# Performance work log

Measured on AMD Instinct MI355X. Metric: run time of the kernel, lower is better.

## Reference

```python
import jax, jax.numpy as jnp
import numpy as np

EPS = 1e-5

def _ln(x, g, b):
    mu = x.mean(-1, keepdims=True)
    var = ((x - mu) ** 2).mean(-1, keepdims=True)
    return (x - mu) / jnp.sqrt(var + EPS) * g + b

def setup_inputs() -> dict:
    key = jax.random.key(0)
    ks = jax.random.split(key, 24)
    B, S, I, H, D, F = 64, 512, 32, 64, 128, 256
    def w(k, shape, fan_in):
        return jax.random.uniform(k, shape, jnp.float32, -1.0, 1.0) / np.sqrt(fan_in)
    return {
        'x': jax.random.normal(ks[0], (B, S, I), jnp.float32),
        'W_ih': w(ks[1], (H, I), H), 'b_ih': w(ks[2], (H,), H),
        'W_hh': w(ks[3], (H, H), H), 'b_hh': w(ks[4], (H,), H),
        'Wp': w(ks[5], (D, H), H), 'bp': w(ks[6], (D,), H),
        'Wqkv': w(ks[7], (3 * D, D), D), 'bqkv': jnp.zeros((3 * D,), jnp.float32),
        'Wo': w(ks[8], (D, D), D), 'bo': jnp.zeros((D,), jnp.float32),
        'g1': jnp.ones((D,), jnp.float32), 'be1': jnp.zeros((D,), jnp.float32),
        'W1': w(ks[9], (F, D), D), 'b1': w(ks[10], (F,), D),
        'W2': w(ks[11], (D, F), F), 'b2': w(ks[12], (D,), F),
        'g2': jnp.ones((D,), jnp.float32), 'be2': jnp.zeros((D,), jnp.float32),
        'gn': jnp.ones((D,), jnp.float32), 'bn': jnp.zeros((D,), jnp.float32),
        'Wf': w(ks[13], (I, D), D), 'bf': w(ks[14], (I,), D),
    }

def reference(x, W_ih, b_ih, W_hh, b_hh, Wp, bp, Wqkv, bqkv, Wo, bo,
              g1, be1, W1, b1, W2, b2, g2, be2, gn, bn, Wf, bf):
    B, S, I = x.shape
    H = W_ih.shape[0]
    D = Wp.shape[0]
    nh = 8
    hd = D // nh

    # RNNCell tanh recurrence over time (sequential, vectorized over batch)
    xs = jnp.swapaxes(x, 0, 1)  # (S, B, I)
    def step(h, x_t):
        h = jnp.tanh(x_t @ W_ih.T + b_ih + h @ W_hh.T + b_hh)
        return h, h
    _, hs = jax.lax.scan(step, jnp.zeros((B, H), x.dtype), xs)  # (S, B, H)

    proj = hs @ Wp.T + bp  # (S, B, D)

    # TransformerEncoderLayer (post-norm, relu), dropout = identity (eval)
    qkv = proj @ Wqkv.T + bqkv  # (S, B, 3D)
    q, k, v = jnp.split(qkv, 3, axis=-1)
    q = q.reshape(S, B, nh, hd)
    k = k.reshape(S, B, nh, hd)
    v = v.reshape(S, B, nh, hd)
    scores = jnp.einsum('sbhd,tbhd->bhst', q, k) / np.sqrt(hd)
    attn = jax.nn.softmax(scores, axis=-1)
    ctx = jnp.einsum('bhst,tbhd->sbhd', attn, v).reshape(S, B, D)
    attn_out = ctx @ Wo.T + bo
    x1 = _ln(proj + attn_out, g1, be1)
    ff = jax.nn.relu(x1 @ W1.T + b1) @ W2.T + b2
    x2 = _ln(x1 + ff, g2, be2)

    out = _ln(x2 + proj, gn, bn)
    pooled = out.mean(axis=0)  # (B, D)
    return jnp.tanh(pooled @ Wf.T + bf)
```

## Files before the change

kernel.cpp:

```cpp
#include <hip/hip_runtime.h>
#include <hip/hip_bf16.h>

#define BB 64
#define SS 512
#define II 32
#define HH 64
#define DD 128
#define FF 256
#define NHEAD 8
#define HDIM 16
#define NTOK (SS*BB)

typedef short bf16x8 __attribute__((ext_vector_type(8)));
typedef float f32x4  __attribute__((ext_vector_type(4)));

__device__ __forceinline__ float fast_tanh(float x) {
    float ax = fabsf(x);
    float e = __expf(-2.0f * ax);
    float r = (1.0f - e) * __builtin_amdgcn_rcpf(1.0f + e);
    return copysignf(r, x);
}

__device__ __forceinline__ float bcast(float v, int lane) {
    return __int_as_float(__builtin_amdgcn_readlane(__float_as_int(v), lane));
}

__device__ __forceinline__ short f2bf(float x) {
    unsigned u = __float_as_uint(x);
    return (short)((u + 0x7FFFu + ((u >> 16) & 1u)) >> 16);
}

__global__ __launch_bounds__(256) void k_xw(const float* __restrict__ x,
                                            const float* __restrict__ W_ih,
                                            const float* __restrict__ b_ih,
                                            const float* __restrict__ b_hh,
                                            float* __restrict__ xw) {
    int idx = blockIdx.x * 256 + threadIdx.x;
    int j  = idx & (HH - 1);
    int sb = idx >> 6;
    int s  = sb >> 6;
    int b  = sb & (BB - 1);
    const float* xr = x + (b * SS + s) * II;
    const float* wr = W_ih + j * II;
    float acc = b_ih[j] + b_hh[j];
    #pragma unroll
    for (int k = 0; k < II; k += 4) {
        float4 xv = *(const float4*)(xr + k);
        float4 wv = *(const float4*)(wr + k);
        acc += xv.x * wv.x + xv.y * wv.y + xv.z * wv.z + xv.w * wv.w;
    }
    xw[idx] = acc;
}

__global__ __launch_bounds__(64, 1) void k_rnn(const float* __restrict__ xw,
                                               const float* __restrict__ W_hh,
                                               float* __restrict__ hs) {
    int b = blockIdx.x;
    int j = threadIdx.x;
    float w[HH];
    #pragma unroll
    for (int k = 0; k < HH; k++) w[k] = W_hh[j * HH + k];

    float hv = 0.0f;
    float xv0 = xw[(0 * BB + b) * HH + j];
    float xv1 = xw[(1 * BB + b) * HH + j];
    for (int t = 0; t < SS; t++) {
        int tn = (t < SS - 2) ? t + 2 : t;
        float xnext = xw[(tn * BB + b) * HH + j];
        float a0 = xv0, a1 = 0.f, a2 = 0.f, a3 = 0.f;
        #pragma unroll
        for (int k = 0; k < HH; k += 4) {
            a0 = fmaf(w[k + 0], bcast(hv, k + 0), a0);
            a1 = fmaf(w[k + 1], bcast(hv, k + 1), a1);
            a2 = fmaf(w[k + 2], bcast(hv, k + 2), a2);
            a3 = fmaf(w[k + 3], bcast(hv, k + 3), a3);
        }
        hv = fast_tanh((a0 + a1) + (a2 + a3));
        hs[(t * BB + b) * HH + j] = hv;
        xv0 = xv1;
        xv1 = xnext;
    }
}

template<int K, bool RELU>
__global__ __launch_bounds__(256) void k_gemm_m64(const float* __restrict__ A,
                                                  const float* __restrict__ W,
                                                  const float* __restrict__ bias,
                                                  float* __restrict__ C, int N) {
    __shared__ short As[64 * 40];
    __shared__ short Ws[128 * 40];
    int tid = threadIdx.x;
    int wid = tid >> 6, lane = tid & 63;
    int col = lane & 15, quad = lane >> 4;
    int rowBase = blockIdx.x * 64, colBase = blockIdx.y * 128;

    f32x4 acc[8];
    #pragma unroll
    for (int nt = 0; nt < 8; nt++) {
        float bv = bias[colBase + nt * 16 + col];
        acc[nt][0] = bv; acc[nt][1] = bv; acc[nt][2] = bv; acc[nt][3] = bv;
    }

    int arow = tid >> 2, akb = (tid & 3) * 8;
    int wrow = tid >> 1, wkb = (tid & 1) * 16;

    for (int kb = 0; kb < K; kb += 32) {
        {
            const float4* ap = (const float4*)(A + (size_t)(rowBase + arow) * K + kb + akb);
            float4 v0 = ap[0], v1 = ap[1];
            short t0[8];
            t0[0]=f2bf(v0.x); t0[1]=f2bf(v0.y); t0[2]=f2bf(v0.z); t0[3]=f2bf(v0.w);
            t0[4]=f2bf(v1.x); t0[5]=f2bf(v1.y); t0[6]=f2bf(v1.z); t0[7]=f2bf(v1.w);
            *(int4*)&As[arow * 40 + akb] = *(int4*)t0;
        }
        {
            const float4* wp = (const float4*)(W + (size_t)(colBase + wrow) * K + kb + wkb);
            float4 v0 = wp[0], v1 = wp[1], v2 = wp[2], v3 = wp[3];
            short t0[8], t1[8];
            t0[0]=f2bf(v0.x); t0[1]=f2bf(v0.y); t0[2]=f2bf(v0.z); t0[3]=f2bf(v0.w);
            t0[4]=f2bf(v1.x); t0[5]=f2bf(v1.y); t0[6]=f2bf(v1.z); t0[7]=f2bf(v1.w);
            t1[0]=f2bf(v2.x); t1[1]=f2bf(v2.y); t1[2]=f2bf(v2.z); t1[3]=f2bf(v2.w);
            t1[4]=f2bf(v3.x); t1[5]=f2bf(v3.y); t1[6]=f2bf(v3.z); t1[7]=f2bf(v3.w);
            *(int4*)&Ws[wrow * 40 + wkb]     = *(int4*)t0;
            *(int4*)&Ws[wrow * 40 + wkb + 8] = *(int4*)t1;
        }
        __syncthreads();

        bf16x8 af = *(const bf16x8*)&As[(wid * 16 + col) * 40 + quad * 8];
        bf16x8 wf[8];
        #pragma unroll
        for (int nt = 0; nt < 8; nt++)
            wf[nt] = *(const bf16x8*)&Ws[(nt * 16 + col) * 40 + quad * 8];
        #pragma unroll
        for (int nt = 0; nt < 8; nt++)
            acc[nt] = __builtin_amdgcn_mfma_f32_16x16x32_bf16(af, wf[nt], acc[nt], 0, 0, 0);
        __syncthreads();
    }

    #pragma unroll
    for (int r = 0; r < 4; r++) {
        int m = rowBase + wid * 16 + quad * 4 + r;
        float* crow = C + (size_t)m * N + colBase;
        #pragma unroll
        for (int nt = 0; nt < 8; nt++) {
            float v = acc[nt][r];
            if (RELU) v = fmaxf(v, 0.f);
            crow[nt * 16 + col] = v;
        }
    }
}

template<int K, int NLN>
__global__ __launch_bounds__(256) void k_gemm_ln_m64(const float* __restrict__ A,
                                                     const float* __restrict__ W,
                                                     const float* __restrict__ bias,
                                                     const float* __restrict__ res1,
                                                     const float* __restrict__ g1v,
                                                     const float* __restrict__ be1v,
                                                     const float* __restrict__ res2,
                                                     const float* __restrict__ g2v,
                                                     const float* __restrict__ be2v,
                                                     float* __restrict__ out) {
    __shared__ short As[64 * 40];
    __shared__ short Ws[128 * 40];
    int tid = threadIdx.x;
    int wid = tid >> 6, lane = tid & 63;
    int col = lane & 15, quad = lane >> 4;
    int rowBase = blockIdx.x * 64;

    f32x4 acc[8];
    #pragma unroll
    for (int nt = 0; nt < 8; nt++) {
        float bv = bias[nt * 16 + col];
        acc[nt][0] = bv; acc[nt][1] = bv; acc[nt][2] = bv; acc[nt][3] = bv;
    }

    int arow = tid >> 2, akb = (tid & 3) * 8;
    int wrow = tid >> 1, wkb = (tid & 1) * 16;

    for (int kb = 0; kb < K; kb += 32) {
        {
            const float4* ap = (const float4*)(A + (size_t)(rowBase + arow) * K + kb + akb);
            float4 v0 = ap[0], v1 = ap[1];
            short t0[8];
            t0[0]=f2bf(v0.x); t0[1]=f2bf(v0.y); t0[2]=f2bf(v0.z); t0[3]=f2bf(v0.w);
            t0[4]=f2bf(v1.x); t0[5]=f2bf(v1.y); t0[6]=f2bf(v1.z); t0[7]=f2bf(v1.w);
            *(int4*)&As[arow * 40 + akb] = *(int4*)t0;
        }
        {
            const float4* wp = (const float4*)(W + (size_t)wrow * K + kb + wkb);
            float4 v0 = wp[0], v1 = wp[1], v2 = wp[2], v3 = wp[3];
            short t0[8], t1[8];
            t0[0]=f2bf(v0.x); t0[1]=f2bf(v0.y); t0[2]=f2bf(v0.z); t0[3]=f2bf(v0.w);
            t0[4]=f2bf(v1.x); t0[5]=f2bf(v1.y); t0[6]=f2bf(v1.z); t0[7]=f2bf(v1.w);
            t1[0]=f2bf(v2.x); t1[1]=f2bf(v2.y); t1[2]=f2bf(v2.z); t1[3]=f2bf(v2.w);
            t1[4]=f2bf(v3.x); t1[5]=f2bf(v3.y); t1[6]=f2bf(v3.z); t1[7]=f2bf(v3.w);
            *(int4*)&Ws[wrow * 40 + wkb]     = *(int4*)t0;
            *(int4*)&Ws[wrow * 40 + wkb + 8] = *(int4*)t1;
        }
        __syncthreads();

        bf16x8 af = *(const bf16x8*)&As[(wid * 16 + col) * 40 + quad * 8];
        bf16x8 wf[8];
        #pragma unroll
        for (int nt = 0; nt < 8; nt++)
            wf[nt] = *(const bf16x8*)&Ws[(nt * 16 + col) * 40 + quad * 8];
        #pragma unroll
        for (int nt = 0; nt < 8; nt++)
            acc[nt] = __builtin_amdgcn_mfma_f32_16x16x32_bf16(af, wf[nt], acc[nt], 0, 0, 0);
        __syncthreads();
    }

    float ga[8], ba[8], gb[8], bb[8];
    #pragma unroll
    for (int nt = 0; nt < 8; nt++) {
        ga[nt] = g1v[nt * 16 + col]; ba[nt] = be1v[nt * 16 + col];
        if (NLN == 2) { gb[nt] = g2v[nt * 16 + col]; bb[nt] = be2v[nt * 16 + col]; }
    }

    #pragma unroll
    for (int r = 0; r < 4; r++) {
        int m = rowBase + wid * 16 + quad * 4 + r;
        const float* rr1 = res1 + (size_t)m * DD;
        float v[8];
        float s = 0.f;
        #pragma unroll
        for (int nt = 0; nt < 8; nt++) {
            v[nt] = acc[nt][r] + rr1[nt * 16 + col];
            s += v[nt];
        }
        #pragma unroll
        for (int off = 1; off < 16; off <<= 1) s += __shfl_xor(s, off, 64);
        float mu = s * (1.0f / 128.0f);
        float vs = 0.f;
        #pragma unroll
        for (int nt = 0; nt < 8; nt++) { v[nt] -= mu; vs += v[nt] * v[nt]; }
        #pragma unroll
        for (int off = 1; off < 16; off <<= 1) vs += __shfl_xor(vs, off, 64);
        float rstd = rsqrtf(vs * (1.0f / 128.0f) + 1e-5f);
        #pragma unroll
        for (int nt = 0; nt < 8; nt++) v[nt] = v[nt] * rstd * ga[nt] + ba[nt];

        if (NLN == 2) {
            const float* rr2 = res2 + (size_t)m * DD;
            float s2 = 0.f;
            #pragma unroll
            for (int nt = 0; nt < 8; nt++) {
                v[nt] += rr2[nt * 16 + col];
                s2 += v[nt];
            }
            #pragma unroll
            for (int off = 1; off < 16; off <<= 1) s2 += __shfl_xor(s2, off, 64);
            float mu2 = s2 * (1.0f / 128.0f);
            float vs2 = 0.f;
            #pragma unroll
            for (int nt = 0; nt < 8; nt++) { v[nt] -= mu2; vs2 += v[nt] * v[nt]; }
            #pragma unroll
            for (int off = 1; off < 16; off <<= 1) vs2 += __shfl_xor(vs2, off, 64);
            float rstd2 = rsqrtf(vs2 * (1.0f / 128.0f) + 1e-5f);
            #pragma unroll
            for (int nt = 0; nt < 8; nt++) v[nt] = v[nt] * rstd2 * gb[nt] + bb[nt];
        }

        float* orow = out + (size_t)m * DD;
        #pragma unroll
        for (int nt = 0; nt < 8; nt++) orow[nt * 16 + col] = v[nt];
    }
}

__global__ __launch_bounds__(256, 2) void k_attn(const float* __restrict__ qkv,
                                                 float* __restrict__ ctx) {
    int bh = blockIdx.x;
    int b = bh >> 3, h = bh & 7;
    __shared__ short Vt[HDIM][SS];
    __shared__ short Pb[4][2][16 * 64];
    int tid = threadIdx.x;

    for (int t = tid; t < SS; t += 256) {
        const float* base = qkv + (size_t)(t * BB + b) * 384 + h * 16;
        float4 v0 = *(const float4*)(base + 256);
        float4 v1 = *(const float4*)(base + 260);
        float4 v2 = *(const float4*)(base + 264);
        float4 v3 = *(const float4*)(base + 268);
        int u = t & 63;
        int pos = (t & ~63) | (((u & 15) << 2) | (u >> 4));
        Vt[0][pos]=f2bf(v0.x);  Vt[1][pos]=f2bf(v0.y);  Vt[2][pos]=f2bf(v0.z);  Vt[3][pos]=f2bf(v0.w);
        Vt[4][pos]=f2bf(v1.x);  Vt[5][pos]=f2bf(v1.y);  Vt[6][pos]=f2bf(v1.z);  Vt[7][pos]=f2bf(v1.w);
        Vt[8][pos]=f2bf(v2.x);  Vt[9][pos]=f2bf(v2.y);  Vt[10][pos]=f2bf(v2.z); Vt[11][pos]=f2bf(v2.w);
        Vt[12][pos]=f2bf(v3.x); Vt[13][pos]=f2bf(v3.y); Vt[14][pos]=f2bf(v3.z); Vt[15][pos]=f2bf(v3.w);
    }
    __syncthreads();

    int wid = tid >> 6, lane = tid & 63;
    int col = lane & 15, quad = lane >> 4;
    const float qscale = 0.25f * 1.44269504f;

    bf16x8 kf[32];
    #pragma unroll
    for (int kt = 0; kt < 32; kt++) {
        bf16x8 f = (bf16x8)(short)0;
        if (quad < 2) {
            const float* ksrc = qkv + (size_t)((kt * 16 + col) * BB + b) * 384 + 128 + h * 16 + quad * 8;
            float4 ka = *(const float4*)ksrc;
            float4 kb2 = *(const float4*)(ksrc + 4);
            f[0]=f2bf(ka.x);  f[1]=f2bf(ka.y);  f[2]=f2bf(ka.z);  f[3]=f2bf(ka.w);
            f[4]=f2bf(kb2.x); f[5]=f2bf(kb2.y); f[6]=f2bf(kb2.z); f[7]=f2bf(kb2.w);
        }
        kf[kt] = f;
    }

    for (int sub = 0; sub < 8; sub++) {
        int q0 = wid * 128 + sub * 16;

        bf16x8 qf = (bf16x8)(short)0;
        if (quad < 2) {
            const float* qsrc = qkv + (size_t)((q0 + col) * BB + b) * 384 + h * 16 + quad * 8;
            float4 qa = *(const float4*)qsrc;
            float4 qb = *(const float4*)(qsrc + 4);
            qf[0]=f2bf(qa.x*qscale); qf[1]=f2bf(qa.y*qscale);
            qf[2]=f2bf(qa.z*qscale); qf[3]=f2bf(qa.w*qscale);
            qf[4]=f2bf(qb.x*qscale); qf[5]=f2bf(qb.y*qscale);
            qf[6]=f2bf(qb.z*qscale); qf[7]=f2bf(qb.w*qscale);
        }

        float l0 = 0.f, l1 = 0.f, l2 = 0.f, l3 = 0.f;
        f32x4 O = {0.f, 0.f, 0.f, 0.f};
        #pragma unroll
        for (int c = 0; c < 8; c++) {
            short* pbuf = &Pb[wid][c & 1][0];
            float p[4][4];
            #pragma unroll
            for (int kk = 0; kk < 4; kk++) {
                f32x4 z = {0.f, 0.f, 0.f, 0.f};
                f32x4 S = __builtin_amdgcn_mfma_f32_16x16x32_bf16(qf, kf[c * 4 + kk], z, 0, 0, 0);
                p[kk][0] = exp2f(S[0]); p[kk][1] = exp2f(S[1]);
                p[kk][2] = exp2f(S[2]); p[kk][3] = exp2f(S[3]);
                l0 += p[kk][0]; l1 += p[kk][1]; l2 += p[kk][2]; l3 += p[kk][3];
            }
            #pragma unroll
            for (int r = 0; r < 4; r++) {
                unsigned w0 = (unsigned)(unsigned short)f2bf(p[0][r])
                            | ((unsigned)(unsigned short)f2bf(p[1][r]) << 16);
                unsigned w1 = (unsigned)(unsigned short)f2bf(p[2][r])
                            | ((unsigned)(unsigned short)f2bf(p[3][r]) << 16);
                *(uint2*)&pbuf[(4 * quad + r) * 64 + col * 4] = make_uint2(w0, w1);
            }
            #pragma unroll
            for (int half = 0; half < 2; half++) {
                int tb = c * 64 + half * 32;
                bf16x8 pf = *(const bf16x8*)&pbuf[col * 64 + half * 32 + quad * 8];
                bf16x8 vf = *(const bf16x8*)&Vt[col][tb + quad * 8];
                O = __builtin_amdgcn_mfma_f32_16x16x32_bf16(pf, vf, O, 0, 0, 0);
            }
        }

        float l[4] = {l0, l1, l2, l3};
        #pragma unroll
        for (int r = 0; r < 4; r++) {
            #pragma unroll
            for (int off = 1; off < 16; off <<= 1) l[r] += __shfl_xor(l[r], off, 64);
            float inv = __builtin_amdgcn_rcpf(l[r]);
            int q = q0 + 4 * quad + r;
            ctx[(size_t)(q * BB + b) * DD + h * 16 + col] = O[r] * inv;
        }
    }
}

__global__ __launch_bounds__(256) void k_poolfinal(const float* __restrict__ outln,
                                                   const float* __restrict__ Wf,
                                                   const float* __restrict__ bfv,
                                                   float* __restrict__ out) {
    int b = blockIdx.x;
    int tid = threadIdx.x;
    __shared__ float part[256];
    __shared__ float pooled[128];
    int d = tid & 127, half = tid >> 7;
    float s = 0.f;
    int s0 = half * 256;
    #pragma unroll 8
    for (int si = s0; si < s0 + 256; si++)
        s += outln[(size_t)(si * BB + b) * DD + d];
    part[tid] = s;
    __syncthreads();
    if (tid < 128) pooled[tid] = (part[tid] + part[tid + 128]) * (1.0f / SS);
    __syncthreads();
    if (tid < 32) {
        const float* wr = Wf + tid * DD;
        float acc = bfv[tid];
        #pragma unroll
        for (int k = 0; k < DD; k += 4) {
            float4 wv = *(const float4*)(wr + k);
            acc += pooled[k] * wv.x + pooled[k + 1] * wv.y
                 + pooled[k + 2] * wv.z + pooled[k + 3] * wv.w;
        }
        out[b * 32 + tid] = fast_tanh(acc);
    }
}

extern "C" void kernel_launch(void* const* d_in, const int* in_sizes, int n_in,
                              void* d_out, int out_size, void* d_ws, size_t ws_size,
                              hipStream_t stream) {
    const float* x    = (const float*)d_in[0];
    const float* W_ih = (const float*)d_in[1];
    const float* b_ih = (const float*)d_in[2];
    const float* W_hh = (const float*)d_in[3];
    const float* b_hh = (const float*)d_in[4];
    const float* Wp   = (const float*)d_in[5];
    const float* bp   = (const float*)d_in[6];
    const float* Wqkv = (const float*)d_in[7];
    const float* bqkv = (const float*)d_in[8];
    const float* Wo   = (const float*)d_in[9];
    const float* bo   = (const float*)d_in[10];
    const float* g1   = (const float*)d_in[11];
    const float* be1  = (const float*)d_in[12];
    const float* W1   = (const float*)d_in[13];
    const float* b1   = (const float*)d_in[14];
    const float* W2   = (const float*)d_in[15];
    const float* b2   = (const float*)d_in[16];
    const float* g2   = (const float*)d_in[17];
    const float* be2  = (const float*)d_in[18];
    const float* gn   = (const float*)d_in[19];
    const float* bn   = (const float*)d_in[20];
    const float* Wf   = (const float*)d_in[21];
    const float* bf   = (const float*)d_in[22];
    float* out = (float*)d_out;
    float* ws  = (float*)d_ws;

    float* proj   = ws + 0;
    float* qkv    = ws + 4194304;
    float* outln  = ws + 4194304;
    float* xw     = ws + 16777216;
    float* hsbuf  = ws + 18874368;
    float* ctx    = ws + 16777216;
    float* x1     = ws + 20971520;
    float* ff1    = ws + 25165824;

    k_xw<<<8192, 256, 0, stream>>>(x, W_ih, b_ih, b_hh, xw);
    k_rnn<<<64, 64, 0, stream>>>(xw, W_hh, hsbuf);
    k_gemm_m64<64,  false><<<dim3(512, 1), 256, 0, stream>>>(hsbuf, Wp, bp, proj, 128);
    k_gemm_m64<128, false><<<dim3(512, 3), 256, 0, stream>>>(proj, Wqkv, bqkv, qkv, 384);
    k_attn<<<512, 256, 0, stream>>>(qkv, ctx);
    k_gemm_ln_m64<128, 1><<<512, 256, 0, stream>>>(ctx, Wo, bo, proj, g1, be1,
                                                   nullptr, nullptr, nullptr, x1);
    k_gemm_m64<128, true ><<<dim3(512, 2), 256, 0, stream>>>(x1, W1, b1, ff1, 256);
    k_gemm_ln_m64<256, 2><<<512, 256, 0, stream>>>(ff1, W2, b2, x1, g2, be2,
                                                   proj, gn, bn, outln);
    k_poolfinal<<<64, 256, 0, stream>>>(outln, Wf, bf, out);
}
```

Baseline: 418.4 us.

## Store intermediate activations and weights in bf16 to halve memory traffic

Intermediate buffers (hidden states, proj, qkv, ctx, x1, ff1) are now written and read as bf16, and a new kernel converts all weight matrices to bf16 once per call, folding the attention scale into the K weights. The GEMM and attention kernels now load bf16 directly into shared memory and registers, with no per-tile fp32-to-bf16 conversion. This is meant to cut global memory traffic and conversion ALU work in the bandwidth-bound stages. The trade-off is an extra launch and more rounding of residuals and activations, which could change accuracy.

```diff
diff --git a/kernel.cpp b/kernel.cpp
--- a/kernel.cpp
+++ b/kernel.cpp
@@ -28,6 +28,30 @@
 __device__ __forceinline__ short f2bf(float x) {
     unsigned u = __float_as_uint(x);
     return (short)((u + 0x7FFFu + ((u >> 16) & 1u)) >> 16);
+}
+__device__ __forceinline__ float bf2f(ushort u) {
+    return __uint_as_float((unsigned)u << 16);
+}
+
+__global__ __launch_bounds__(256) void k_wcvt(const float* __restrict__ Wp,
+                                              const float* __restrict__ Wqkv,
+                                              const float* __restrict__ Wo,
+                                              const float* __restrict__ W1,
+                                              const float* __restrict__ W2,
+                                              ushort* __restrict__ out) {
+    int i = blockIdx.x * 256 + threadIdx.x;
+    float v;
+    if (i < 8192) v = Wp[i];
+    else if (i < 57344) {
+        int e = i - 8192;
+        v = Wqkv[e];
+        int row = e >> 7;
+        if (row >= 128 && row < 256) v *= 0.36067376f;
+    }
+    else if (i < 73728) v = Wo[i - 57344];
+    else if (i < 106496) v = W1[i - 73728];
+    else v = W2[i - 106496];
+    out[i] = (ushort)f2bf(v);
 }
 
 __global__ __launch_bounds__(256) void k_xw(const float* __restrict__ x,
@@ -54,7 +78,7 @@
 
 __global__ __launch_bounds__(64, 1) void k_rnn(const float* __restrict__ xw,
                                                const float* __restrict__ W_hh,
-                                               float* __restrict__ hs) {
+                                               ushort* __restrict__ hs) {
     int b = blockIdx.x;
     int j = threadIdx.x;
     float w[HH];
@@ -76,17 +100,17 @@
             a3 = fmaf(w[k + 3], bcast(hv, k + 3), a3);
         }
         hv = fast_tanh((a0 + a1) + (a2 + a3));
-        hs[(t * BB + b) * HH + j] = hv;
+        hs[(t * BB + b) * HH + j] = (ushort)f2bf(hv);
         xv0 = xv1;
         xv1 = xnext;
     }
 }
 
-template<int K, bool RELU>
-__global__ __launch_bounds__(256) void k_gemm_m64(const float* __restrict__ A,
-                                                  const float* __restrict__ W,
-                                                  const float* __restrict__ bias,
-                                                  float* __restrict__ C, int N) {
+template<int K, bool RELU, bool OUTBF>
+__global__ __launch_bounds__(256) void k_gemm_m64b(const ushort* __restrict__ A,
+                                                   const ushort* __restrict__ W,
+                                                   const float* __restrict__ bias,
+                                                   void* __restrict__ Cv, int N) {
     __shared__ short As[64 * 40];
     __shared__ short Ws[128 * 40];
     int tid = threadIdx.x;
@@ -101,28 +125,16 @@
         acc[nt][0] = bv; acc[nt][1] = bv; acc[nt][2] = bv; acc[nt][3] = bv;
     }
 
-    int arow = tid >> 2, akb = (tid & 3) * 8;
-    int wrow = tid >> 1, wkb = (tid & 1) * 16;
+    int arow = tid >> 2, akc = (tid & 3) * 8;
+    int wrow = tid >> 1, wkc = (tid & 1) * 16;
 
     for (int kb = 0; kb < K; kb += 32) {
+        *(int4*)&As[arow * 40 + akc] =
+            *(const int4*)(A + (size_t)(rowBase + arow) * K + kb + akc);
         {
-            const float4* ap = (const float4*)(A + (size_t)(rowBase + arow) * K + kb + akb);
-            float4 v0 = ap[0], v1 = ap[1];
-            short t0[8];
-            t0[0]=f2bf(v0.x); t0[1]=f2bf(v0.y); t0[2]=f2bf(v0.z); t0[3]=f2bf(v0.w);
-            t0[4]=f2bf(v1.x); t0[5]=f2bf(v1.y); t0[6]=f2bf(v1.z); t0[7]=f2bf(v1.w);
-            *(int4*)&As[arow * 40 + akb] = *(int4*)t0;
-        }
-        {
-            const float4* wp = (const float4*)(W + (size_t)(colBase + wrow) * K + kb + wkb);
-            float4 v0 = wp[0], v1 = wp[1], v2 = wp[2], v3 = wp[3];
-            short t0[8], t1[8];
-            t0[0]=f2bf(v0.x); t0[1]=f2bf(v0.y); t0[2]=f2bf(v0.z); t0[3]=f2bf(v0.w);
-            t0[4]=f2bf(v1.x); t0[5]=f2bf(v1.y); t0[6]=f2bf(v1.z); t0[7]=f2bf(v1.w);
-            t1[0]=f2bf(v2.x); t1[1]=f2bf(v2.y); t1[2]=f2bf(v2.z); t1[3]=f2bf(v2.w);
-            t1[4]=f2bf(v3.x); t1[5]=f2bf(v3.y); t1[6]=f2bf(v3.z); t1[7]=f2bf(v3.w);
-            *(int4*)&Ws[wrow * 40 + wkb]     = *(int4*)t0;
-            *(int4*)&Ws[wrow * 40 + wkb + 8] = *(int4*)t1;
+            const int4* wp = (const int4*)(W + (size_t)(colBase + wrow) * K + kb + wkc);
+            *(int4*)&Ws[wrow * 40 + wkc]     = wp[0];
+            *(int4*)&Ws[wrow * 40 + wkc + 8] = wp[1];
         }
         __syncthreads();
 
@@ -140,27 +152,29 @@
     #pragma unroll
     for (int r = 0; r < 4; r++) {
         int m = rowBase + wid * 16 + quad * 4 + r;
-        float* crow = C + (size_t)m * N + colBase;
         #pragma unroll
         for (int nt = 0; nt < 8; nt++) {
             float v = acc[nt][r];
             if (RELU) v = fmaxf(v, 0.f);
-            crow[nt * 16 + col] = v;
-        }
-    }
-}
-
-template<int K, int NLN>
-__global__ __launch_bounds__(256) void k_gemm_ln_m64(const float* __restrict__ A,
-                                                     const float* __restrict__ W,
-                                                     const float* __restrict__ bias,
-                                                     const float* __restrict__ res1,
-                                                     const float* __restrict__ g1v,
-                                                     const float* __restrict__ be1v,
-                                                     const float* __restrict__ res2,
-                                                     const float* __restrict__ g2v,
-                                                     const float* __restrict__ be2v,
-                                                     float* __restrict__ out) {
+            if (OUTBF)
+                ((ushort*)Cv)[(size_t)m * N + colBase + nt * 16 + col] = (ushort)f2bf(v);
+            else
+                ((float*)Cv)[(size_t)m * N + colBase + nt * 16 + col] = v;
+        }
+    }
+}
+
+template<int K, int NLN, bool OUTBF>
+__global__ __launch_bounds__(256) void k_gemm_ln_m64b(const ushort* __restrict__ A,
+                                                      const ushort* __restrict__ W,
+                                                      const float* __restrict__ bias,
+                                                      const ushort* __restrict__ res1,
+                                                      const float* __restrict__ g1v,
+                                                      const float* __restrict__ be1v,
+                                                      const ushort* __restrict__ res2,
+                                                      const float* __restrict__ g2v,
+                                                      const float* __restrict__ be2v,
+                                                      void* __restrict__ outv) {
     __shared__ short As[64 * 40];
     __shared__ short Ws[128 * 40];
     int tid = threadIdx.x;
@@ -175,28 +189,16 @@
         acc[nt][0] = bv; acc[nt][1] = bv; acc[nt][2] = bv; acc[nt][3] = bv;
     }
 
-    int arow = tid >> 2, akb = (tid & 3) * 8;
-    int wrow = tid >> 1, wkb = (tid & 1) * 16;
+    int arow = tid >> 2, akc = (tid & 3) * 8;
+    int wrow = tid >> 1, wkc = (tid & 1) * 16;
 
     for (int kb = 0; kb < K; kb += 32) {
+        *(int4*)&As[arow * 40 + akc] =
+            *(const int4*)(A + (size_t)(rowBase + arow) * K + kb + akc);
         {
-            const float4* ap = (const float4*)(A + (size_t)(rowBase + arow) * K + kb + akb);
-            float4 v0 = ap[0], v1 = ap[1];
-            short t0[8];
-            t0[0]=f2bf(v0.x); t0[1]=f2bf(v0.y); t0[2]=f2bf(v0.z); t0[3]=f2bf(v0.w);
-            t0[4]=f2bf(v1.x); t0[5]=f2bf(v1.y); t0[6]=f2bf(v1.z); t0[7]=f2bf(v1.w);
-            *(int4*)&As[arow * 40 + akb] = *(int4*)t0;
-        }
-        {
-            const float4* wp = (const float4*)(W + (size_t)wrow * K + kb + wkb);
-            float4 v0 = wp[0], v1 = wp[1], v2 = wp[2], v3 = wp[3];
-            short t0[8], t1[8];
-            t0[0]=f2bf(v0.x); t0[1]=f2bf(v0.y); t0[2]=f2bf(v0.z); t0[3]=f2bf(v0.w);
-            t0[4]=f2bf(v1.x); t0[5]=f2bf(v1.y); t0[6]=f2bf(v1.z); t0[7]=f2bf(v1.w);
-            t1[0]=f2bf(v2.x); t1[1]=f2bf(v2.y); t1[2]=f2bf(v2.z); t1[3]=f2bf(v2.w);
-            t1[4]=f2bf(v3.x); t1[5]=f2bf(v3.y); t1[6]=f2bf(v3.z); t1[7]=f2bf(v3.w);
-            *(int4*)&Ws[wrow * 40 + wkb]     = *(int4*)t0;
-            *(int4*)&Ws[wrow * 40 + wkb + 8] = *(int4*)t1;
+            const int4* wp = (const int4*)(W + (size_t)wrow * K + kb + wkc);
+            *(int4*)&Ws[wrow * 40 + wkc]     = wp[0];
+            *(int4*)&Ws[wrow * 40 + wkc + 8] = wp[1];
         }
         __syncthreads();
 
@@ -221,12 +223,12 @@
     #pragma unroll
     for (int r = 0; r < 4; r++) {
         int m = rowBase + wid * 16 + quad * 4 + r;
-        const float* rr1 = res1 + (size_t)m * DD;
+        const ushort* rr1 = res1 + (size_t)m * DD;
         float v[8];
         float s = 0.f;
         #pragma unroll
         for (int nt = 0; nt < 8; nt++) {
-            v[nt] = acc[nt][r] + rr1[nt * 16 + col];
+            v[nt] = acc[nt][r] + bf2f(rr1[nt * 16 + col]);
             s += v[nt];
         }
         #pragma unroll
@@ -242,11 +244,11 @@
         for (int nt = 0; nt < 8; nt++) v[nt] = v[nt] * rstd * ga[nt] + ba[nt];
 
         if (NLN == 2) {
-            const float* rr2 = res2 + (size_t)m * DD;
+            const ushort* rr2 = res2 + (size_t)m * DD;
             float s2 = 0.f;
             #pragma unroll
             for (int nt = 0; nt < 8; nt++) {
-                v[nt] += rr2[nt * 16 + col];
+                v[nt] += bf2f(rr2[nt * 16 + col]);
                 s2 += v[nt];
             }
             #pragma unroll
@@ -262,14 +264,18 @@
             for (int nt = 0; nt < 8; nt++) v[nt] = v[nt] * rstd2 * gb[nt] + bb[nt];
         }
 
-        float* orow = out + (size_t)m * DD;
-        #pragma unroll
-        for (int nt = 0; nt < 8; nt++) orow[nt * 16 + col] = v[nt];
-    }
-}
-
-__global__ __launch_bounds__(256, 2) void k_attn(const float* __restrict__ qkv,
-                                                 float* __restrict__ ctx) {
+        #pragma unroll
+        for (int nt = 0; nt < 8; nt++) {
+            if (OUTBF)
+                ((ushort*)outv)[(size_t)m * DD + nt * 16 + col] = (ushort)f2bf(v[nt]);
+            else
+                ((float*)outv)[(size_t)m * DD + nt * 16 + col] = v[nt];
+        }
+    }
+}
+
+__global__ __launch_bounds__(256, 2) void k_attn(const ushort* __restrict__ qkv,
+                                                 ushort* __restrict__ ctx) {
     int bh = blockIdx.x;
     int b = bh >> 3, h = bh & 7;
     __shared__ short Vt[HDIM][SS];
@@ -277,35 +283,31 @@
     int tid = threadIdx.x;
 
     for (int t = tid; t < SS; t += 256) {
-        const float* base = qkv + (size_t)(t * BB + b) * 384 + h * 16;
-        float4 v0 = *(const float4*)(base + 256);
-        float4 v1 = *(const float4*)(base + 260);
-        float4 v2 = *(const float4*)(base + 264);
-        float4 v3 = *(const float4*)(base + 268);
+        const ushort* base = qkv + (size_t)(t * BB + b) * 384 + 256 + h * 16;
+        int4 va = *(const int4*)base;
+        int4 vb = *(const int4*)(base + 8);
+        const ushort* pa = (const ushort*)&va;
+        const ushort* pb = (const ushort*)&vb;
         int u = t & 63;
         int pos = (t & ~63) | (((u & 15) << 2) | (u >> 4));
-        Vt[0][pos]=f2bf(v0.x);  Vt[1][pos]=f2bf(v0.y);  Vt[2][pos]=f2bf(v0.z);  Vt[3][pos]=f2bf(v0.w);
-        Vt[4][pos]=f2bf(v1.x);  Vt[5][pos]=f2bf(v1.y);  Vt[6][pos]=f2bf(v1.z);  Vt[7][pos]=f2bf(v1.w);
-        Vt[8][pos]=f2bf(v2.x);  Vt[9][pos]=f2bf(v2.y);  Vt[10][pos]=f2bf(v2.z); Vt[11][pos]=f2bf(v2.w);
-        Vt[12][pos]=f2bf(v3.x); Vt[13][pos]=f2bf(v3.y); Vt[14][pos]=f2bf(v3.z); Vt[15][pos]=f2bf(v3.w);
+        #pragma unroll
+        for (int d = 0; d < 8; d++) {
+            Vt[d][pos]     = pa[d];
+            Vt[d + 8][pos] = pb[d];
+        }
     }
     __syncthreads();
 
     int wid = tid >> 6, lane = tid & 63;
     int col = lane & 15, quad = lane >> 4;
-    const float qscale = 0.25f * 1.44269504f;
 
     bf16x8 kf[32];
     #pragma unroll
     for (int kt = 0; kt < 32; kt++) {
         bf16x8 f = (bf16x8)(short)0;
-        if (quad < 2) {
-            const float* ksrc = qkv + (size_t)((kt * 16 + col) * BB + b) * 384 + 128 + h * 16 + quad * 8;
-            float4 ka = *(const float4*)ksrc;
-            float4 kb2 = *(const float4*)(ksrc + 4);
-            f[0]=f2bf(ka.x);  f[1]=f2bf(ka.y);  f[2]=f2bf(ka.z);  f[3]=f2bf(ka.w);
-            f[4]=f2bf(kb2.x); f[5]=f2bf(kb2.y); f[6]=f2bf(kb2.z); f[7]=f2bf(kb2.w);
-        }
+        if (quad < 2)
+            f = *(const bf16x8*)(qkv + (size_t)((kt * 16 + col) * BB + b) * 384
+                                 + 128 + h * 16 + quad * 8);
         kf[kt] = f;
     }
 
@@ -313,15 +315,9 @@
         int q0 = wid * 128 + sub * 16;
 
         bf16x8 qf = (bf16x8)(short)0;
-        if (quad < 2) {
-            const float* qsrc = qkv + (size_t)((q0 + col) * BB + b) * 384 + h * 16 + quad * 8;
-            float4 qa = *(const float4*)qsrc;
-            float4 qb = *(const float4*)(qsrc + 4);
-            qf[0]=f2bf(qa.x*qscale); qf[1]=f2bf(qa.y*qscale);
-            qf[2]=f2bf(qa.z*qscale); qf[3]=f2bf(qa.w*qscale);
-            qf[4]=f2bf(qb.x*qscale); qf[5]=f2bf(qb.y*qscale);
-            qf[6]=f2bf(qb.z*qscale); qf[7]=f2bf(qb.w*qscale);
-        }
+        if (quad < 2)
+            qf = *(const bf16x8*)(qkv + (size_t)((q0 + col) * BB + b) * 384
+                                  + h * 16 + quad * 8);
 
         float l0 = 0.f, l1 = 0.f, l2 = 0.f, l3 = 0.f;
         f32x4 O = {0.f, 0.f, 0.f, 0.f};
@@ -361,7 +357,7 @@
             for (int off = 1; off < 16; off <<= 1) l[r] += __shfl_xor(l[r], off, 64);
             float inv = __builtin_amdgcn_rcpf(l[r]);
             int q = q0 + 4 * quad + r;
-            ctx[(size_t)(q * BB + b) * DD + h * 16 + col] = O[r] * inv;
+            ctx[(size_t)(q * BB + b) * DD + h * 16 + col] = (ushort)f2bf(O[r] * inv);
         }
     }
 }
@@ -424,26 +420,33 @@
     const float* Wf   = (const float*)d_in[21];
     const float* bf   = (const float*)d_in[22];
     float* out = (float*)d_out;
-    float* ws  = (float*)d_ws;
-
-    float* proj   = ws + 0;
-    float* qkv    = ws + 4194304;
-    float* outln  = ws + 4194304;
-    float* xw     = ws + 16777216;
-    float* hsbuf  = ws + 18874368;
-    float* ctx    = ws + 16777216;
-    float* x1     = ws + 20971520;
-    float* ff1    = ws + 25165824;
-
+    char* wsb = (char*)d_ws;
+
+    float*  xw    = (float*)(wsb);
+    ushort* hsb   = (ushort*)(wsb + (8u << 20));
+    ushort* projb = (ushort*)(wsb + (12u << 20));
+    ushort* qkvb  = (ushort*)(wsb + (20u << 20));
+    ushort* ctxb  = (ushort*)(wsb + (44u << 20));
+    ushort* x1b   = (ushort*)(wsb + (52u << 20));
+    ushort* ff1b  = (ushort*)(wsb + (60u << 20));
+    float*  outln = (float*)(wsb + (76u << 20));
+    ushort* wbf   = (ushort*)(wsb + (92u << 20));
+    ushort* Wp_bf   = wbf;
+    ushort* Wqkv_bf = wbf + 8192;
+    ushort* Wo_bf   = wbf + 57344;
+    ushort* W1_bf   = wbf + 73728;
+    ushort* W2_bf   = wbf + 106496;
+
+    k_wcvt<<<544, 256, 0, stream>>>(Wp, Wqkv, Wo, W1, W2, wbf);
     k_xw<<<8192, 256, 0, stream>>>(x, W_ih, b_ih, b_hh, xw);
-    k_rnn<<<64, 64, 0, stream>>>(xw, W_hh, hsbuf);
-    k_gemm_m64<64,  false><<<dim3(512, 1), 256, 0, stream>>>(hsbuf, Wp, bp, proj, 128);
-    k_gemm_m64<128, false><<<dim3(512, 3), 256, 0, stream>>>(proj, Wqkv, bqkv, qkv, 384);
-    k_attn<<<512, 256, 0, stream>>>(qkv, ctx);
-    k_gemm_ln_m64<128, 1><<<512, 256, 0, stream>>>(ctx, Wo, bo, proj, g1, be1,
-                                                   nullptr, nullptr, nullptr, x1);
-    k_gemm_m64<128, true ><<<dim3(512, 2), 256, 0, stream>>>(x1, W1, b1, ff1, 256);
-    k_gemm_ln_m64<256, 2><<<512, 256, 0, stream>>>(ff1, W2, b2, x1, g2, be2,
-                                                   proj, gn, bn, outln);
+    k_rnn<<<64, 64, 0, stream>>>(xw, W_hh, hsb);
+    k_gemm_m64b<64,  false, true><<<dim3(512, 1), 256, 0, stream>>>(hsb, Wp_bf, bp, projb, 128);
+    k_gemm_m64b<128, false, true><<<dim3(512, 3), 256, 0, stream>>>(projb, Wqkv_bf, bqkv, qkvb, 384);
+    k_attn<<<512, 256, 0, stream>>>(qkvb, ctxb);
+    k_gemm_ln_m64b<128, 1, true><<<512, 256, 0, stream>>>(ctxb, Wo_bf, bo, projb, g1, be1,
+                                                          nullptr, nullptr, nullptr, x1b);
+    k_gemm_m64b<128, true, true><<<dim3(512, 2), 256, 0, stream>>>(x1b, W1_bf, b1, ff1b, 256);
+    k_gemm_ln_m64b<256, 2, false><<<512, 256, 0, stream>>>(ff1b, W2_bf, b2, x1b, g2, be2,
+                                                           projb, gn, bn, outln);
     k_poolfinal<<<64, 256, 0, stream>>>(outln, Wf, bf, out);
 }
```

New measurement: 405.7 us. 1.03x faster.
